# Kernel optimization log

Hardware: AMD Instinct MI355X
Metric: run time of the kernel (lower is better)

The kernel has to match this reference:

```python
import jax, jax.numpy as jnp
import numpy as np

# Architecture constants (match init_kwargs)
A = 4            # num_areas
E_PER = 512      # excitatory units per area
I_PER = 128      # inhibitory units per area
H = A * (E_PER + I_PER)   # 2560 hidden units, order: [all E (area-major), all I]
NUM_OBJS = 2
IN_UNITS = 64
IN = NUM_OBJS * IN_UNITS  # 128 input units
DT, TAU_X = 0.02, 0.1
ALPHA_X = DT / TAU_X


def _build_masks():
    """Signed Dale's-law connectivity masks, as in _get_connectivity_mask_* ."""
    # inter-area recurrent connectivity: nearest-neighbor hierarchy + self
    rec = np.eye(A) + np.eye(A, k=1) + np.eye(A, k=-1)
    ee = np.kron(rec, np.ones((E_PER, E_PER)))
    ei = np.kron(np.eye(A), np.ones((E_PER, I_PER)))   # E<-I only within area
    ie = np.kron(rec, np.ones((I_PER, E_PER)))
    ii = np.kron(np.eye(A), np.ones((I_PER, I_PER)))
    conn = np.block([[ee, ei], [ie, ii]])
    # sign mask: first e_size columns excitatory (+1), rest inhibitory (-1)
    sign = np.concatenate([np.ones(A * E_PER), -np.ones(A * I_PER)])[None, :]
    rec_mask = conn * sign
    np.fill_diagonal(rec_mask, 0.0)  # remove_diag=True in h2h EILinear
    # input mask: only area 0 receives external input; e_prop=1 for x2h (all +1)
    in_area = np.zeros((A, NUM_OBJS)); in_area[0, :] = 1.0
    in_e = np.kron(in_area, np.ones((E_PER, IN_UNITS)))
    in_i = np.kron(in_area, np.ones((I_PER, IN_UNITS)))
    in_mask = np.concatenate([in_e, in_i], axis=0)
    return jnp.asarray(rec_mask, jnp.float32), jnp.asarray(in_mask, jnp.float32)


def setup_inputs() -> dict:
    key = jax.random.key(0)
    k1, k2, k3 = jax.random.split(key, 3)
    T, B = 500, 64
    inputs = jax.random.normal(k1, (T, B, IN), dtype=jnp.float32)
    W_rec = jax.random.normal(k2, (H, H), dtype=jnp.float32) / np.sqrt(H)
    b_rec = jnp.zeros((H,), dtype=jnp.float32)
    W_in = jax.random.normal(k3, (H, IN), dtype=jnp.float32) / np.sqrt(IN)
    return {"inputs": inputs, "W_rec": W_rec, "b_rec": b_rec, "W_in": W_in}


def reference(inputs, W_rec, b_rec, W_in):
    rec_mask, in_mask = _build_masks()
    # EILinear effective weights: pos_func=abs, times signed connectivity mask
    W_rec_eff = jnp.abs(W_rec) * rec_mask          # [H, H]
    W_in_eff = jnp.abs(W_in) * in_mask             # [H, IN]
    # input projection for all timesteps at once
    proj = jnp.einsum('tbi,hi->tbh', inputs, W_in_eff)  # [T, B, H]

    def retanh(x):
        return jnp.tanh(jax.nn.relu(x))

    def step(carry, u_t):
        x, r = carry
        pre = r @ W_rec_eff.T + b_rec + u_t        # h2h(r) + x2h(u)
        x = (1.0 - ALPHA_X) * x + ALPHA_X * pre    # leaky integration
        r = retanh(x)
        return (x, r), r

    B = inputs.shape[1]
    x0 = jnp.zeros((B, H), dtype=inputs.dtype)     # x0 (train_init_state=False)
    (_, _), rates = jax.lax.scan(step, (x0, retanh(x0)), proj)
    return rates  # [T, B, H] firing rates
```

## Files before the change

### kernel.cpp

```cpp
#include <hip/hip_runtime.h>
#include <math.h>

#define Hn   2560
#define Bn   64
#define INW  128
#define ETOT 2048
#define HGn  160
#define MAXC 13
#define NBLK 160
#define MAXI 7

typedef __attribute__((ext_vector_type(8))) _Float16 half8;
typedef __attribute__((ext_vector_type(4))) float  floatx4;

__global__ void build_apack(const float* __restrict__ Wrec,
                            const float* __restrict__ Win,
                            _Float16* __restrict__ Af) {
  int hg = blockIdx.x, c = blockIdx.y;
  int a = (hg < 128) ? (hg >> 5) : ((hg - 128) >> 3);
  int nE = (a == 0 || a == 3) ? 8 : 12;
  int nch = nE + 1 + (a == 0 ? 1 : 0);
  if (c >= nch) return;
  int h0 = hg * 16;
  int tid = threadIdx.x;
  int kq = tid >> 6, L = tid & 63;
  int m = L & 15, q = L >> 4;
  int h = h0 + m;

  const float* src; int k0, stride; float sgn; bool isIn = false;
  if (c < nE)       { k0 = ((a == 0 ? 0 : a - 1) << 9) + (c << 7); src = Wrec; stride = Hn;  sgn =  1.f; }
  else if (c == nE) { k0 = ETOT + (a << 7);                        src = Wrec; stride = Hn;  sgn = -1.f; }
  else              { k0 = 0;                                      src = Win;  stride = INW; sgn =  1.f; isIn = true; }

  _Float16 hi8[8], lo8[8];
  #pragma unroll
  for (int j = 0; j < 8; ++j) {
    int k = k0 + kq * 32 + q * 8 + j;
    float w = fabsf(src[(size_t)h * stride + k]);
    if (!isIn && k == h) w = 0.f;
    w *= sgn;
    _Float16 wh = (_Float16)w;
    hi8[j] = wh;
    lo8[j] = (_Float16)(w - (float)wh);
  }
  _Float16* outp = Af + (size_t)(hg * MAXC + c) * 4096;
  *(uint4*)(outp + (kq * 2 + 0) * 512 + L * 8) = *(const uint4*)hi8;
  *(uint4*)(outp + (kq * 2 + 1) * 512 + L * 8) = *(const uint4*)lo8;
}

#define LOAD4(B0,B1,B2,B3,P) \
  asm volatile("global_load_dwordx4 %0, %4, off sc0 sc1\n\t" \
               "global_load_dwordx4 %1, %4, off offset:1024 sc0 sc1\n\t" \
               "global_load_dwordx4 %2, %4, off offset:2048 sc0 sc1\n\t" \
               "global_load_dwordx4 %3, %4, off offset:3072 sc0 sc1\n\t" \
               "s_waitcnt vmcnt(0)" \
               : "=&v"(B0), "=&v"(B1), "=&v"(B2), "=&v"(B3) \
               : "v"(P) : "memory")

#define LOAD8(X0,X1,X2,X3,Y0,Y1,Y2,Y3,PA,PB) \
  asm volatile("global_load_dwordx4 %0, %8, off sc0 sc1\n\t" \
               "global_load_dwordx4 %1, %8, off offset:1024 sc0 sc1\n\t" \
               "global_load_dwordx4 %2, %8, off offset:2048 sc0 sc1\n\t" \
               "global_load_dwordx4 %3, %8, off offset:3072 sc0 sc1\n\t" \
               "global_load_dwordx4 %4, %9, off sc0 sc1\n\t" \
               "global_load_dwordx4 %5, %9, off offset:1024 sc0 sc1\n\t" \
               "global_load_dwordx4 %6, %9, off offset:2048 sc0 sc1\n\t" \
               "global_load_dwordx4 %7, %9, off offset:3072 sc0 sc1\n\t" \
               "s_waitcnt vmcnt(0)" \
               : "=&v"(X0), "=&v"(X1), "=&v"(X2), "=&v"(X3), \
                 "=&v"(Y0), "=&v"(Y1), "=&v"(Y2), "=&v"(Y3) \
               : "v"(PA), "v"(PB) : "memory")

#define MFMA8(i, B0,B1,B2,B3) do { \
  ac0 = __builtin_amdgcn_mfma_f32_16x16x32_f16(ah[i], B0, ac0, 0, 0, 0); \
  ac0 = __builtin_amdgcn_mfma_f32_16x16x32_f16(al[i], B0, ac0, 0, 0, 0); \
  ac1 = __builtin_amdgcn_mfma_f32_16x16x32_f16(ah[i], B1, ac1, 0, 0, 0); \
  ac1 = __builtin_amdgcn_mfma_f32_16x16x32_f16(al[i], B1, ac1, 0, 0, 0); \
  ac2 = __builtin_amdgcn_mfma_f32_16x16x32_f16(ah[i], B2, ac2, 0, 0, 0); \
  ac2 = __builtin_amdgcn_mfma_f32_16x16x32_f16(al[i], B2, ac2, 0, 0, 0); \
  ac3 = __builtin_amdgcn_mfma_f32_16x16x32_f16(ah[i], B3, ac3, 0, 0, 0); \
  ac3 = __builtin_amdgcn_mfma_f32_16x16x32_f16(al[i], B3, ac3, 0, 0, 0); \
} while (0)

#define RECPATH1(i) do { \
  half8 B0_, B1_, B2_, B3_; \
  const _Float16* pp_ = rs + boff[i]; \
  LOAD4(B0_, B1_, B2_, B3_, pp_); \
  MFMA8(i, B0_, B1_, B2_, B3_); \
} while (0)

#define INPATH(i) do { \
  const float* ip_ = inputs + (size_t)t * (Bn * INW) + boff[i]; \
  int nb_ = L & 15; \
  half8 B0_, B1_, B2_, B3_; \
  _Pragma("unroll") for (int j = 0; j < 8; ++j) B0_[j] = (_Float16)ip_[(nb_ +  0) * INW + j]; \
  _Pragma("unroll") for (int j = 0; j < 8; ++j) B1_[j] = (_Float16)ip_[(nb_ + 16) * INW + j]; \
  _Pragma("unroll") for (int j = 0; j < 8; ++j) B2_[j] = (_Float16)ip_[(nb_ + 32) * INW + j]; \
  _Pragma("unroll") for (int j = 0; j < 8; ++j) B3_[j] = (_Float16)ip_[(nb_ + 48) * INW + j]; \
  MFMA8(i, B0_, B1_, B2_, B3_); \
} while (0)

#define PAIR(i0, i1) do { \
  bool r0_ = act[i0] && !isin[i0]; \
  bool r1_ = act[i1] && !isin[i1]; \
  if (r0_ && r1_) { \
    half8 X0_,X1_,X2_,X3_,Y0_,Y1_,Y2_,Y3_; \
    const _Float16* pa_ = rs + boff[i0]; \
    const _Float16* pb_ = rs + boff[i1]; \
    LOAD8(X0_,X1_,X2_,X3_,Y0_,Y1_,Y2_,Y3_, pa_, pb_); \
    MFMA8(i0, X0_, X1_, X2_, X3_); \
    MFMA8(i1, Y0_, Y1_, Y2_, Y3_); \
  } else { \
    if (r0_) RECPATH1(i0); else if (act[i0]) INPATH(i0); \
    if (r1_) RECPATH1(i1); else if (act[i1]) INPATH(i1); \
  } \
} while (0)

__global__ __launch_bounds__(512, 2) void rnn_persist(
    const _Float16* __restrict__ Af,
    const float* __restrict__ inputs,
    _Float16* __restrict__ rfA, _Float16* __restrict__ rfB,
    const float* __restrict__ brec,
    float* __restrict__ rates,
    unsigned* bar, int T)
{
  __shared__ float red[8][1056];
  __shared__ float rrt[16][68];
  __shared__ float bb[16];

  const int hg  = blockIdx.x;
  const int tid = threadIdx.x;
  const int w   = tid >> 6, L = tid & 63;
  const int h0  = hg * 16;
  const int a   = (hg < 128) ? (hg >> 5) : ((hg - 128) >> 3);
  const int nE  = (a == 0 || a == 3) ? 8 : 12;
  const int SK  = (nE + 1 + (a == 0 ? 1 : 0)) * 4;
  const int ktE0 = (a == 0 ? 0 : a - 1) * 16;
  const int ktI0 = 64 + a * 4;

  unsigned* bsub = bar + (hg & 7) * 64;
  unsigned* bmas = bar + 8 * 64;
  unsigned* bgen = bar + 9 * 64;

  if (tid < 16) bb[tid] = brec[h0 + tid];

  half8 ah[MAXI], al[MAXI];
  int   boff[MAXI];
  bool  act[MAXI], isin[MAXI];
  const _Float16* Abase = Af + (size_t)hg * MAXC * 4096;
  #pragma unroll
  for (int i = 0; i < MAXI; ++i) {
    half8 zz = {0,0,0,0,0,0,0,0};
    ah[i] = zz; al[i] = zz;
    int ks = w + i * 8;
    act[i]  = ks < SK;
    isin[i] = false;
    boff[i] = 0;
    if (act[i]) {
      int c = ks >> 2, kq = ks & 3;
      const _Float16* Ap = Abase + (size_t)c * 4096 + (size_t)(kq * 2) * 512 + (size_t)L * 8;
      ah[i] = *(const half8*)Ap;
      al[i] = *(const half8*)(Ap + 512);
      if (c <= nE) {
        int kt = (c < nE) ? (ktE0 + c * 4 + kq) : (ktI0 + kq);
        boff[i] = kt * 2048 + L * 8;
      } else {
        isin[i] = true;
        boff[i] = kq * 32 + (L >> 4) * 8;
      }
    }
  }
  #pragma unroll
  for (int i = 0; i < MAXI; ++i)
    asm volatile("" : "+v"(ah[i]), "+v"(al[i]));

  float xv[2] = {0.f, 0.f};

  __syncthreads();

  for (int t = 0; t < T; ++t) {
    const _Float16* __restrict__ rs = (t & 1) ? rfB : rfA;
    _Float16* __restrict__ rd       = (t & 1) ? rfA : rfB;

    floatx4 ac0 = {0.f,0.f,0.f,0.f}, ac1 = {0.f,0.f,0.f,0.f};
    floatx4 ac2 = {0.f,0.f,0.f,0.f}, ac3 = {0.f,0.f,0.f,0.f};

    PAIR(0, 1);
    PAIR(2, 3);
    PAIR(4, 5);
    if (act[6]) { if (!isin[6]) RECPATH1(6); else INPATH(6); }

    #pragma unroll
    for (int p = 0; p < 4; ++p) {
      int m = (L >> 4) * 4 + p;
      float* rw = &red[w][m * 66 + (L & 15)];
      rw[ 0] = ac0[p];
      rw[16] = ac1[p];
      rw[32] = ac2[p];
      rw[48] = ac3[p];
    }
    __syncthreads();

    #pragma unroll
    for (int e = 0; e < 2; ++e) {
      int elem = tid + e * 512;
      int m = elem >> 6, n = elem & 63;
      float s = 0.f;
      #pragma unroll
      for (int j = 0; j < 8; ++j) s += red[j][m * 66 + n];
      float x = 0.8f * xv[e] + 0.2f * (s + bb[m]);
      xv[e] = x;
      rrt[m][n] = tanhf(fmaxf(x, 0.f));
    }
    __syncthreads();

    if (tid < 128) {
      int bt = tid >> 5, Lq = tid & 31;
      int Lp = (hg & 1) * 32 + Lq;
      half8 vv;
      #pragma unroll
      for (int j = 0; j < 8; ++j)
        vv[j] = (_Float16)rrt[(Lq >> 4) * 8 + j][bt * 16 + (Lq & 15)];
      _Float16* dst = rd + (size_t)((hg >> 1) * 4 + bt) * 512 + (size_t)Lp * 8;
      asm volatile("global_store_dwordx4 %0, %1, off sc0 sc1\n\t"
                   "s_waitcnt vmcnt(0)"
                   :: "v"(dst), "v"(vv) : "memory");
    }
    if (tid >= 256) {
      int tt = tid - 256;
      int b = tt >> 2, hq = tt & 3;
      floatx4 o;
      o.x = rrt[hq * 4 + 0][b];
      o.y = rrt[hq * 4 + 1][b];
      o.z = rrt[hq * 4 + 2][b];
      o.w = rrt[hq * 4 + 3][b];
      __builtin_nontemporal_store(o,
          (floatx4*)(rates + (size_t)t * (Bn * Hn) + (size_t)b * Hn + h0 + hq * 4));
    }
    __syncthreads();

    if (t + 1 < T) {
      if (tid == 0) {
        unsigned g = (unsigned)(t + 1);
        bool done = false;
        unsigned s = __hip_atomic_fetch_add(bsub, 1u, __ATOMIC_RELAXED,
                                            __HIP_MEMORY_SCOPE_AGENT);
        if (s == g * 20u - 1u) {
          unsigned m2 = __hip_atomic_fetch_add(bmas, 1u, __ATOMIC_RELAXED,
                                               __HIP_MEMORY_SCOPE_AGENT);
          if (m2 == g * 8u - 1u) {
            __hip_atomic_store(bgen, g, __ATOMIC_RELAXED,
                               __HIP_MEMORY_SCOPE_AGENT);
            done = true;
          }
        }
        if (!done) {
          while (__hip_atomic_load(bgen, __ATOMIC_RELAXED,
                                   __HIP_MEMORY_SCOPE_AGENT) < g)
            __builtin_amdgcn_s_sleep(2);
        }
      }
      __syncthreads();
    }
  }
}

extern "C" void kernel_launch(void* const* d_in, const int* in_sizes, int n_in,
                              void* d_out, int out_size, void* d_ws, size_t ws_size,
                              hipStream_t stream) {
  const float* inputs = (const float*)d_in[0];
  const float* Wrec   = (const float*)d_in[1];
  const float* brec   = (const float*)d_in[2];
  const float* Win    = (const float*)d_in[3];
  int T = in_sizes[0] / (Bn * INW);

  char* base = (char*)d_ws;
  size_t off = 0;
  _Float16* Af  = (_Float16*)(base + off); off += (size_t)HGn * MAXC * 4096 * 2;
  _Float16* rfA = (_Float16*)(base + off); off += (size_t)80 * 4 * 512 * 2;
  _Float16* rfB = (_Float16*)(base + off); off += (size_t)80 * 4 * 512 * 2;
  unsigned* bar = (unsigned*)(base + off); off += 4096;

  (void)hipMemsetAsync(rfA, 0, (size_t)80 * 4 * 512 * 2, stream);
  (void)hipMemsetAsync(bar, 0, 4096, stream);

  build_apack<<<dim3(HGn, MAXC), 256, 0, stream>>>(Wrec, Win, Af);

  float* rates = (float*)d_out;
  rnn_persist<<<NBLK, 512, 0, stream>>>(Af, inputs, rfA, rfB, brec, rates,
                                        bar, T);
}
```

Baseline: 2.856 ms.

## Batch all recurrent loads before MFMAs and simplify the grid barrier to polling the master counter

Input-path MFMAs now run first. All recurrent-state loads for every k-slice are then issued together behind a single vmcnt wait, instead of waiting per pair, so memory latency overlaps across slices. The two-level barrier drops its generation flag and every block polls the master counter directly, which removes one atomic store from the critical path but makes all 160 blocks spin on one contended address. Launch bounds go from 2 to 1 block per SM to give the buffered B fragments more registers, at the cost of occupancy.

```diff
diff --git a/kernel.cpp b/kernel.cpp
--- a/kernel.cpp
+++ b/kernel.cpp
@@ -48,28 +48,13 @@
   *(uint4*)(outp + (kq * 2 + 1) * 512 + L * 8) = *(const uint4*)lo8;
 }
 
-#define LOAD4(B0,B1,B2,B3,P) \
+#define LOADI(B0,B1,B2,B3,P) \
   asm volatile("global_load_dwordx4 %0, %4, off sc0 sc1\n\t" \
                "global_load_dwordx4 %1, %4, off offset:1024 sc0 sc1\n\t" \
                "global_load_dwordx4 %2, %4, off offset:2048 sc0 sc1\n\t" \
-               "global_load_dwordx4 %3, %4, off offset:3072 sc0 sc1\n\t" \
-               "s_waitcnt vmcnt(0)" \
+               "global_load_dwordx4 %3, %4, off offset:3072 sc0 sc1" \
                : "=&v"(B0), "=&v"(B1), "=&v"(B2), "=&v"(B3) \
                : "v"(P) : "memory")
-
-#define LOAD8(X0,X1,X2,X3,Y0,Y1,Y2,Y3,PA,PB) \
-  asm volatile("global_load_dwordx4 %0, %8, off sc0 sc1\n\t" \
-               "global_load_dwordx4 %1, %8, off offset:1024 sc0 sc1\n\t" \
-               "global_load_dwordx4 %2, %8, off offset:2048 sc0 sc1\n\t" \
-               "global_load_dwordx4 %3, %8, off offset:3072 sc0 sc1\n\t" \
-               "global_load_dwordx4 %4, %9, off sc0 sc1\n\t" \
-               "global_load_dwordx4 %5, %9, off offset:1024 sc0 sc1\n\t" \
-               "global_load_dwordx4 %6, %9, off offset:2048 sc0 sc1\n\t" \
-               "global_load_dwordx4 %7, %9, off offset:3072 sc0 sc1\n\t" \
-               "s_waitcnt vmcnt(0)" \
-               : "=&v"(X0), "=&v"(X1), "=&v"(X2), "=&v"(X3), \
-                 "=&v"(Y0), "=&v"(Y1), "=&v"(Y2), "=&v"(Y3) \
-               : "v"(PA), "v"(PB) : "memory")
 
 #define MFMA8(i, B0,B1,B2,B3) do { \
   ac0 = __builtin_amdgcn_mfma_f32_16x16x32_f16(ah[i], B0, ac0, 0, 0, 0); \
@@ -82,41 +67,7 @@
   ac3 = __builtin_amdgcn_mfma_f32_16x16x32_f16(al[i], B3, ac3, 0, 0, 0); \
 } while (0)
 
-#define RECPATH1(i) do { \
-  half8 B0_, B1_, B2_, B3_; \
-  const _Float16* pp_ = rs + boff[i]; \
-  LOAD4(B0_, B1_, B2_, B3_, pp_); \
-  MFMA8(i, B0_, B1_, B2_, B3_); \
-} while (0)
-
-#define INPATH(i) do { \
-  const float* ip_ = inputs + (size_t)t * (Bn * INW) + boff[i]; \
-  int nb_ = L & 15; \
-  half8 B0_, B1_, B2_, B3_; \
-  _Pragma("unroll") for (int j = 0; j < 8; ++j) B0_[j] = (_Float16)ip_[(nb_ +  0) * INW + j]; \
-  _Pragma("unroll") for (int j = 0; j < 8; ++j) B1_[j] = (_Float16)ip_[(nb_ + 16) * INW + j]; \
-  _Pragma("unroll") for (int j = 0; j < 8; ++j) B2_[j] = (_Float16)ip_[(nb_ + 32) * INW + j]; \
-  _Pragma("unroll") for (int j = 0; j < 8; ++j) B3_[j] = (_Float16)ip_[(nb_ + 48) * INW + j]; \
-  MFMA8(i, B0_, B1_, B2_, B3_); \
-} while (0)
-
-#define PAIR(i0, i1) do { \
-  bool r0_ = act[i0] && !isin[i0]; \
-  bool r1_ = act[i1] && !isin[i1]; \
-  if (r0_ && r1_) { \
-    half8 X0_,X1_,X2_,X3_,Y0_,Y1_,Y2_,Y3_; \
-    const _Float16* pa_ = rs + boff[i0]; \
-    const _Float16* pb_ = rs + boff[i1]; \
-    LOAD8(X0_,X1_,X2_,X3_,Y0_,Y1_,Y2_,Y3_, pa_, pb_); \
-    MFMA8(i0, X0_, X1_, X2_, X3_); \
-    MFMA8(i1, Y0_, Y1_, Y2_, Y3_); \
-  } else { \
-    if (r0_) RECPATH1(i0); else if (act[i0]) INPATH(i0); \
-    if (r1_) RECPATH1(i1); else if (act[i1]) INPATH(i1); \
-  } \
-} while (0)
-
-__global__ __launch_bounds__(512, 2) void rnn_persist(
+__global__ __launch_bounds__(512, 1) void rnn_persist(
     const _Float16* __restrict__ Af,
     const float* __restrict__ inputs,
     _Float16* __restrict__ rfA, _Float16* __restrict__ rfB,
@@ -140,7 +91,6 @@
 
   unsigned* bsub = bar + (hg & 7) * 64;
   unsigned* bmas = bar + 8 * 64;
-  unsigned* bgen = bar + 9 * 64;
 
   if (tid < 16) bb[tid] = brec[h0 + tid];
 
@@ -185,10 +135,40 @@
     floatx4 ac0 = {0.f,0.f,0.f,0.f}, ac1 = {0.f,0.f,0.f,0.f};
     floatx4 ac2 = {0.f,0.f,0.f,0.f}, ac3 = {0.f,0.f,0.f,0.f};
 
-    PAIR(0, 1);
-    PAIR(2, 3);
-    PAIR(4, 5);
-    if (act[6]) { if (!isin[6]) RECPATH1(6); else INPATH(6); }
+    #pragma unroll
+    for (int i = 0; i < MAXI; ++i) {
+      if (act[i] && isin[i]) {
+        const float* ip = inputs + (size_t)t * (Bn * INW) + boff[i];
+        int nb = L & 15;
+        half8 b0, b1, b2, b3;
+        #pragma unroll
+        for (int j = 0; j < 8; ++j) b0[j] = (_Float16)ip[(nb +  0) * INW + j];
+        #pragma unroll
+        for (int j = 0; j < 8; ++j) b1[j] = (_Float16)ip[(nb + 16) * INW + j];
+        #pragma unroll
+        for (int j = 0; j < 8; ++j) b2[j] = (_Float16)ip[(nb + 32) * INW + j];
+        #pragma unroll
+        for (int j = 0; j < 8; ++j) b3[j] = (_Float16)ip[(nb + 48) * INW + j];
+        MFMA8(i, b0, b1, b2, b3);
+      }
+    }
+
+    half8 Bv0[MAXI], Bv1[MAXI], Bv2[MAXI], Bv3[MAXI];
+    #pragma unroll
+    for (int i = 0; i < MAXI; ++i) {
+      if (act[i] && !isin[i]) {
+        const _Float16* p = rs + boff[i];
+        LOADI(Bv0[i], Bv1[i], Bv2[i], Bv3[i], p);
+      }
+    }
+    asm volatile("s_waitcnt vmcnt(0)" ::: "memory");
+    __builtin_amdgcn_sched_barrier(0);
+
+    #pragma unroll
+    for (int i = 0; i < MAXI; ++i) {
+      if (act[i] && !isin[i])
+        MFMA8(i, Bv0[i], Bv1[i], Bv2[i], Bv3[i]);
+    }
 
     #pragma unroll
     for (int p = 0; p < 4; ++p) {
@@ -242,23 +222,14 @@
     if (t + 1 < T) {
       if (tid == 0) {
         unsigned g = (unsigned)(t + 1);
-        bool done = false;
         unsigned s = __hip_atomic_fetch_add(bsub, 1u, __ATOMIC_RELAXED,
                                             __HIP_MEMORY_SCOPE_AGENT);
-        if (s == g * 20u - 1u) {
-          unsigned m2 = __hip_atomic_fetch_add(bmas, 1u, __ATOMIC_RELAXED,
-                                               __HIP_MEMORY_SCOPE_AGENT);
-          if (m2 == g * 8u - 1u) {
-            __hip_atomic_store(bgen, g, __ATOMIC_RELAXED,
-                               __HIP_MEMORY_SCOPE_AGENT);
-            done = true;
-          }
-        }
-        if (!done) {
-          while (__hip_atomic_load(bgen, __ATOMIC_RELAXED,
-                                   __HIP_MEMORY_SCOPE_AGENT) < g)
-            __builtin_amdgcn_s_sleep(2);
-        }
+        if (s == g * 20u - 1u)
+          __hip_atomic_fetch_add(bmas, 1u, __ATOMIC_RELAXED,
+                                 __HIP_MEMORY_SCOPE_AGENT);
+        while (__hip_atomic_load(bmas, __ATOMIC_RELAXED,
+                                 __HIP_MEMORY_SCOPE_AGENT) < g * 8u)
+          __builtin_amdgcn_s_sleep(2);
       }
       __syncthreads();
     }
```

Result: slower. 3.217 ms (+12.6%).
